# Kernel tuning notes

Measured on AMD Instinct MI355X. Metric: run time of the kernel, lower is better.

Reference implementation:

```python
import jax, jax.numpy as jnp
import numpy as np

T_TOK, N_UNITS, E, H, L_PATH, N_PATHS, B, VOCAB = 16, 4096, 128, 128, 32, 1024, 8, 16384
MAX_PATH_LEN = 32
PAD_ID = 0


def _run_lstm(x, Wi, Wh, b):
    # x: [T, N, E]; torch gate order i, f, g, o
    Hh = Wh.shape[1]
    h0 = jnp.zeros((x.shape[1], Hh), x.dtype)
    def step(carry, xt):
        h, c = carry
        g = xt @ Wi.T + h @ Wh.T + b
        i, f, gg, o = jnp.split(g, 4, axis=-1)
        c = jax.nn.sigmoid(f) * c + jax.nn.sigmoid(i) * jnp.tanh(gg)
        h = jax.nn.sigmoid(o) * jnp.tanh(c)
        return (h, c), h
    _, ys = jax.lax.scan(step, (h0, h0), x)
    return ys


def _bilstm(x, lengths, Wif, Whf, bf, Wib, Whb, bb):
    # emulates pack_padded_sequence + bidirectional LSTM + pad_packed (zeros past length)
    T = x.shape[0]
    t = jnp.arange(T)[:, None]
    valid = t < lengths[None, :]
    out_f = _run_lstm(x, Wif, Whf, bf)
    rev = jnp.clip(lengths[None, :] - 1 - t, 0, T - 1)  # reverse within each valid prefix
    x_rev = jnp.take_along_axis(x, rev[:, :, None], axis=0)
    out_b = jnp.take_along_axis(_run_lstm(x_rev, Wib, Whb, bb), rev[:, :, None], axis=0)
    return jnp.concatenate([out_f, out_b], axis=-1) * valid[:, :, None]


def _layernorm(x, g, b):
    m = x.mean(-1, keepdims=True)
    v = ((x - m) ** 2).mean(-1, keepdims=True)
    return (x - m) * jax.lax.rsqrt(v + 1e-5) * g + b


def _forward(units, paths, unit_per_data, path_per_data, emb, tl_Wif, tl_Whf, tl_bf,
             tl_Wib, tl_Whb, tl_bb, lin_W, lin_b, ln_g, ln_b, attn_w, attn_b,
             pl_Wif, pl_Whf, pl_bf, pl_Wib, pl_Whb, pl_bb, ul_W, ul_b):
    # ---- _token_encoder ----
    is_pad = units == PAD_ID
    tok_len = jnp.where(is_pad.any(0), jnp.argmax(is_pad, 0), units.shape[0])
    x = emb[units]                                              # [T, NU, E]
    h = _bilstm(x, tok_len, tl_Wif, tl_Whf, tl_bf, tl_Wib, tl_Whb, tl_bb)  # [T, NU, 2H]
    out = h @ lin_W.T + lin_b                                   # [T, NU, E]
    q = jnp.tanh(_layernorm(out, ln_g, ln_b))
    scores = q @ attn_w.T + attn_b                              # [T, NU, 1] local attention
    scores = jnp.where(is_pad[:, :, None], -1e9, scores)
    w = jax.nn.softmax(scores, axis=0)
    tok_feat = jnp.einsum('tn,tne->ne', w[..., 0], out)         # [NU, E]
    # ---- _unit_to_path (vectorized ragged gather) ----
    Lp, Pn = paths.shape
    has_end = (paths == -1).any(0)
    fe = jnp.where(has_end, jnp.argmax(paths == -1, 0), Lp)
    ML = min(Lp, MAX_PATH_LEN)
    nb = unit_per_data.shape[0]
    data_of_path = jnp.repeat(jnp.arange(nb), path_per_data, total_repeat_length=Pn)
    u_off = jnp.cumsum(unit_per_data) - unit_per_data
    off_p = u_off[data_of_path]
    un_p = unit_per_data[data_of_path]
    pL = paths[:ML]
    t = jnp.arange(ML)[:, None]
    within = t < fe[None, :]
    keep = within & (pL >= 0) & (pL < un_p[None, :])
    gidx = jnp.clip(jnp.clip(pL, 0, None) + off_p[None, :], 0, tok_feat.shape[0] - 1)
    feats = tok_feat[gidx] * keep[:, :, None]                   # [ML, P, E]
    mask = jnp.where(within, (pL < 0) | (pL > un_p[None, :]), True)
    # ---- _path_encoder ----
    p_len = jnp.where(mask.any(0), jnp.argmax(mask, 0), ML)
    hp = _bilstm(feats, p_len, pl_Wif, pl_Whf, pl_bf, pl_Wib, pl_Whb, pl_bb)
    return hp @ ul_W.T + ul_b                                   # [ML, P, E]


def setup_inputs() -> dict:
    rng = np.random.default_rng(0)
    tok_len = rng.integers(4, T_TOK + 1, N_UNITS); tok_len[0] = T_TOK
    units = rng.integers(1, VOCAB, (T_TOK, N_UNITS))
    units = np.where(np.arange(T_TOK)[:, None] < tok_len[None, :], units, PAD_ID)
    upd = N_UNITS // B
    p_len = rng.integers(8, L_PATH + 1, N_PATHS); p_len[0] = L_PATH
    paths = rng.integers(0, upd, (L_PATH, N_PATHS))
    paths = np.where(np.arange(L_PATH)[:, None] < p_len[None, :], paths, -1)
    key = jax.random.key(0)
    ks = iter(jax.random.split(key, 24))
    def pn(shape, s=0.08):
        return (jax.random.normal(next(ks), shape) * s).astype(jnp.float32)
    return dict(
        units=jnp.asarray(units, jnp.int32),
        paths=jnp.asarray(paths, jnp.int32),
        unit_per_data=jnp.full((B,), upd, jnp.int32),
        path_per_data=jnp.full((B,), N_PATHS // B, jnp.int32),
        emb=pn((VOCAB, E)),
        tl_Wif=pn((4 * H, E)), tl_Whf=pn((4 * H, H)), tl_bf=pn((4 * H,)),
        tl_Wib=pn((4 * H, E)), tl_Whb=pn((4 * H, H)), tl_bb=pn((4 * H,)),
        lin_W=pn((E, 2 * H)), lin_b=pn((E,)),
        ln_g=jnp.ones((E,), jnp.float32), ln_b=jnp.zeros((E,), jnp.float32),
        attn_w=pn((1, E)), attn_b=pn((1,)),
        pl_Wif=pn((4 * H, E)), pl_Whf=pn((4 * H, H)), pl_bf=pn((4 * H,)),
        pl_Wib=pn((4 * H, E)), pl_Whb=pn((4 * H, H)), pl_bb=pn((4 * H,)),
        ul_W=pn((E, 2 * H)), ul_b=pn((E,)),
    )


def reference(units, paths, unit_per_data, path_per_data, emb, tl_Wif, tl_Whf, tl_bf,
              tl_Wib, tl_Whb, tl_bb, lin_W, lin_b, ln_g, ln_b, attn_w, attn_b,
              pl_Wif, pl_Whf, pl_bf, pl_Wib, pl_Whb, pl_bb, ul_W, ul_b):
    return _forward(units, paths, unit_per_data, path_per_data, emb, tl_Wif, tl_Whf, tl_bf,
                    tl_Wib, tl_Whb, tl_bb, lin_W, lin_b, ln_g, ln_b, attn_w, attn_b,
                    pl_Wif, pl_Whf, pl_bf, pl_Wib, pl_Whb, pl_bb, ul_W, ul_b)
```

## Files before the change

kernel.cpp:

```cpp
#include <hip/hip_runtime.h>
#include <cstdint>
#include <cstddef>

#define T_TOKN 16
#define NUNITS 4096
#define LPATH  32
#define NPATHS 1024
#define BNUM   8

typedef __attribute__((ext_vector_type(8))) short short8;
typedef __attribute__((ext_vector_type(4))) short short4x;
typedef __attribute__((ext_vector_type(4))) float f32x4;

enum : size_t {
  OFF_WFRAG   = 0,
  OFF_LINFRAG = 262144,
  OFF_OUTF    = 294912,
  OFF_OUTB    = OFF_OUTF + 4194304,
  OFF_OUTLIN  = OFF_OUTB + 4194304,
  OFF_SCORES  = OFF_OUTLIN + 8388608,
  OFF_TOKFEAT = OFF_SCORES + 65536,
  OFF_POUTF   = OFF_TOKFEAT + 524288,
  OFF_POUTB   = OFF_POUTF + 2097152,
  OFF_INT     = OFF_POUTB + 2097152,
  WS_FLOATS   = OFF_INT + 8192
};

static __device__ __forceinline__ unsigned short f2bf(float f) {
  union { float f; unsigned u; } v; v.f = f;
  unsigned r = v.u + 0x7fffu + ((v.u >> 16) & 1u);
  return (unsigned short)(r >> 16);
}
static __device__ __forceinline__ unsigned pack_bf(float a, float b) {
  return (unsigned)f2bf(a) | ((unsigned)f2bf(b) << 16);
}
static __device__ __forceinline__ float sigf(float x)      { return 1.f / (1.f + __expf(-x)); }
static __device__ __forceinline__ float tanhfast(float x)  { return 2.f / (1.f + __expf(-2.f * x)) - 1.f; }

__global__ void prep_kernel(
    const float* __restrict__ tWif, const float* __restrict__ tWhf,
    const float* __restrict__ tWib, const float* __restrict__ tWhb,
    const float* __restrict__ pWif, const float* __restrict__ pWhf,
    const float* __restrict__ pWib, const float* __restrict__ pWhb,
    const float* __restrict__ linW, const float* __restrict__ ulW,
    const int* __restrict__ units, const int* __restrict__ paths,
    const int* __restrict__ upd, const int* __restrict__ ppd,
    float* __restrict__ ws, int* __restrict__ ip)
{
  int idx = blockIdx.x * 256 + threadIdx.x;
  if (idx < 524288) {
    unsigned short* wf = (unsigned short*)(ws + OFF_WFRAG);
    int mat = idx >> 17, rem = idx & 131071;
    int i  = rem & 7;
    int lane = (rem >> 3) & 63;
    int ct = (rem >> 9) & 3;
    int ks = (rem >> 11) & 7;
    int wv = (rem >> 14) & 7;
    int g = wv * 64 + ct * 16 + (lane & 15);
    int k = ks * 32 + ((lane >> 4) << 3) + i;
    const float* Wi; const float* Wh;
    switch (mat) {
      case 0: Wi = tWif; Wh = tWhf; break;
      case 1: Wi = tWib; Wh = tWhb; break;
      case 2: Wi = pWif; Wh = pWhf; break;
      default: Wi = pWib; Wh = pWhb; break;
    }
    float v = (k < 128) ? Wi[g * 128 + k] : Wh[g * 128 + (k - 128)];
    wf[idx] = f2bf(v);
  } else if (idx < 524288 + 65536) {
    unsigned short* lf = (unsigned short*)(ws + OFF_LINFRAG);
    int i2 = idx - 524288;
    int mat = i2 >> 15, rem = i2 & 32767;
    int i  = rem & 7;
    int lane = (rem >> 3) & 63;
    int ks = (rem >> 9) & 7;
    int ct = (rem >> 12) & 7;
    int e = ct * 16 + (lane & 15);
    int k = ks * 32 + ((lane >> 4) << 3) + i;
    const float* W = mat ? ulW : linW;
    lf[i2] = f2bf(W[e * 256 + k]);
  } else if (idx < 589824 + 4096) {
    int n = idx - 589824;
    int len = T_TOKN;
    for (int t = 0; t < T_TOKN; ++t)
      if (units[t * NUNITS + n] == 0) { len = t; break; }
    ip[n] = len;
  } else if (idx < 589824 + 5120) {
    int p = idx - (589824 + 4096);
    int* fe_a  = ip + 4096;
    int* p_len = ip + 5120;
    int* off_p = ip + 6144;
    int* un_p  = ip + 7168;
    int cum = 0; int d = BNUM - 1;
    for (int dd = 0; dd < BNUM; ++dd) {
      int c2 = cum + ppd[dd];
      if (p < c2) { d = dd; break; }
      cum = c2;
    }
    int off = 0;
    for (int dd = 0; dd < d; ++dd) off += upd[dd];
    int un = upd[d];
    off_p[p] = off; un_p[p] = un;
    int f = LPATH;
    for (int t = 0; t < LPATH; ++t)
      if (paths[t * NPATHS + p] == -1) { f = t; break; }
    fe_a[p] = f;
    int pl = LPATH;
    for (int t = 0; t < LPATH; ++t) {
      int v = paths[t * NPATHS + p];
      if ((t >= f) || (v < 0) || (v > un)) { pl = t; break; }
    }
    p_len[p] = pl;
  }
}

template <int MODE>
__global__ __launch_bounds__(1024, 4) void lstm_kernel(
    const unsigned short* __restrict__ wfragAll,
    const float* __restrict__ biasF, const float* __restrict__ biasB,
    const float* __restrict__ src,
    const int* __restrict__ idxsrc,
    const int* __restrict__ lens,
    const int* __restrict__ fe_a, const int* __restrict__ off_p, const int* __restrict__ un_p,
    unsigned short* __restrict__ outF, unsigned short* __restrict__ outB)
{
  constexpr int NN   = MODE ? NPATHS : NUNITS;
  constexpr int TT   = MODE ? LPATH : T_TOKN;
  constexpr int M    = MODE ? 8 : 32;
  constexpr int MR   = MODE ? 16 : 32;
  constexpr int NRT  = MR / 16;
  constexpr int ASTR = 264;
  constexpr int GSTR = 514;

  __shared__ unsigned short ash[MR * ASTR];
  __shared__ float gates[MR * GSTR];
  __shared__ int   idxL[M * TT];

  int tid  = threadIdx.x;
  int dir  = blockIdx.y;
  int n0   = blockIdx.x * M;
  int lane = tid & 63, wv = tid >> 6;

  const unsigned short* wbase =
      wfragAll + (size_t)((MODE ? 2 : 0) + dir) * 131072;
  int wv8 = wv >> 1;
  short8 bfr[8][2];
#pragma unroll
  for (int ks = 0; ks < 8; ++ks)
#pragma unroll
    for (int c2 = 0; c2 < 2; ++c2) {
      int ct = ((wv & 1) << 1) | c2;
      bfr[ks][c2] = *(const short8*)&wbase[((((wv8 * 8 + ks) * 4 + ct) * 64) + lane) * 8];
    }

  if (MODE == 0) {
    for (int i = tid; i < MR * 128; i += 1024)
      ash[(i >> 7) * ASTR + 128 + (i & 127)] = 0;
  } else {
    for (int i = tid; i < MR * ASTR; i += 1024) ash[i] = 0;
  }
  for (int i = tid; i < M * TT; i += 1024) {
    int u = i / TT, tt = i - u * TT;
    idxL[i] = idxsrc[tt * NN + (n0 + u)];
  }

  const float* bcp = dir ? biasB : biasF;
  int j2 = MODE ? (tid & 127) : ((tid & 63) * 2);
  int ug = MODE ? (tid >> 7)  : (tid >> 6);
  float2 b2[4];
#pragma unroll
  for (int q = 0; q < 4; ++q) {
    if (MODE == 0) b2[q] = *(const float2*)&bcp[q * 128 + j2];
    else           b2[q] = make_float2(bcp[q * 128 + j2], 0.f);
  }
  constexpr int NU = MODE ? 1 : 2;
  float cst0[NU], cst1[NU];
  int   ulen[NU];
  unsigned hp_prev[NU];
#pragma unroll
  for (int i = 0; i < NU; ++i) {
    cst0[i] = 0.f; cst1[i] = 0.f;
    ulen[i] = lens[n0 + ug * NU + i];
    hp_prev[i] = 0u;
  }

  int gu, gk0;
  if (MODE == 0) { gu = tid >> 5; gk0 = (tid & 31) * 4; }
  else           { gu = tid >> 7; gk0 = tid & 127; }
  int gn = n0 + gu;
  int glen = lens[gn];
  int gfe = 0, goff = 0, gun = 0;
  if (MODE) { gfe = fe_a[gn]; goff = off_p[gn]; gun = un_p[gn]; }

  float4 xq; float xs;
  __syncthreads();

  {
    int tau = dir ? min(max(glen - 1, 0), TT - 1) : 0;
    int v = idxL[gu * TT + tau];
    if (MODE == 0) {
      xq = *(const float4*)&src[(size_t)v * 128 + gk0];
    } else {
      bool keep = (tau < gfe) && (v >= 0) && (v < gun);
      xs = keep ? src[(size_t)min(v + goff, NUNITS - 1) * 128 + gk0] : 0.f;
    }
  }
  if (MODE == 0) {
    short4x x4;
    x4[0] = (short)f2bf(xq.x); x4[1] = (short)f2bf(xq.y);
    x4[2] = (short)f2bf(xq.z); x4[3] = (short)f2bf(xq.w);
    *(short4x*)&ash[gu * ASTR + gk0] = x4;
  } else {
    ash[gu * ASTR + gk0] = f2bf(xs);
  }
  __syncthreads();

#pragma unroll 1
  for (int t = 0; t < TT; ++t) {
    if (t > 0) {
      int tpw = t - 1;
#pragma unroll
      for (int i = 0; i < NU; ++i) {
        int u = ug * NU + i, n = n0 + u, L = ulen[i];
        bool vld = tpw < L;
        if (MODE == 0) {
          if (dir == 0) {
            *(unsigned*)&outF[((size_t)tpw * NN + n) * 128 + j2] = hp_prev[i];
          } else {
            size_t tr = vld ? (size_t)(L - 1 - tpw) : (size_t)tpw;
            *(unsigned*)&outB[(tr * NN + n) * 128 + j2] = vld ? hp_prev[i] : 0u;
          }
        } else {
          unsigned short hb = (unsigned short)hp_prev[i];
          if (dir == 0) {
            outF[((size_t)tpw * NN + n) * 128 + j2] = hb;
          } else {
            size_t tr = vld ? (size_t)(L - 1 - tpw) : (size_t)tpw;
            outB[(tr * NN + n) * 128 + j2] = vld ? hb : (unsigned short)0;
          }
        }
      }
    }
    {
      int tn = (t + 1 < TT) ? t + 1 : t;
      int taun = dir ? min(max(glen - 1 - tn, 0), TT - 1) : tn;
      int vn = idxL[gu * TT + taun];
      if (MODE == 0) {
        xq = *(const float4*)&src[(size_t)vn * 128 + gk0];
      } else {
        bool keep = (taun < gfe) && (vn >= 0) && (vn < gun);
        xs = keep ? src[(size_t)min(vn + goff, NUNITS - 1) * 128 + gk0] : 0.f;
      }
    }
    {
      f32x4 acc[NRT][2];
#pragma unroll
      for (int rt = 0; rt < NRT; ++rt)
#pragma unroll
        for (int c2 = 0; c2 < 2; ++c2) {
          f32x4 z = {0.f, 0.f, 0.f, 0.f};
          acc[rt][c2] = z;
        }
#pragma unroll
      for (int ks = 0; ks < 8; ++ks) {
        short8 afr[NRT];
#pragma unroll
        for (int rt = 0; rt < NRT; ++rt)
          afr[rt] = *(const short8*)&ash[(rt * 16 + (lane & 15)) * ASTR + ks * 32 + ((lane >> 4) << 3)];
#pragma unroll
        for (int rt = 0; rt < NRT; ++rt)
#pragma unroll
          for (int c2 = 0; c2 < 2; ++c2)
            acc[rt][c2] = __builtin_amdgcn_mfma_f32_16x16x32_bf16(
                afr[rt], bfr[ks][c2], acc[rt][c2], 0, 0, 0);
      }
#pragma unroll
      for (int rt = 0; rt < NRT; ++rt)
#pragma unroll
        for (int c2 = 0; c2 < 2; ++c2) {
          int g = wv * 32 + c2 * 16 + (lane & 15);
#pragma unroll
          for (int r = 0; r < 4; ++r) {
            int u = rt * 16 + ((lane >> 4) << 2) + r;
            gates[u * GSTR + g] = acc[rt][c2][r];
          }
        }
    }
    __syncthreads();

#pragma unroll
    for (int i = 0; i < NU; ++i) {
      int u = ug * NU + i;
      int L = ulen[i];
      if (t < L) {
        if (MODE == 0) {
          float2 g0 = *(const float2*)&gates[u * GSTR + j2];
          float2 g1 = *(const float2*)&gates[u * GSTR + 128 + j2];
          float2 g2 = *(const float2*)&gates[u * GSTR + 256 + j2];
          float2 g3 = *(const float2*)&gates[u * GSTR + 384 + j2];
          float i0 = sigf(g0.x + b2[0].x), i1 = sigf(g0.y + b2[0].y);
          float f0 = sigf(g1.x + b2[1].x), f1 = sigf(g1.y + b2[1].y);
          float c0 = tanhfast(g2.x + b2[2].x), c1 = tanhfast(g2.y + b2[2].y);
          float o0 = sigf(g3.x + b2[3].x), o1 = sigf(g3.y + b2[3].y);
          float cA = f0 * cst0[i] + i0 * c0;
          float cB = f1 * cst1[i] + i1 * c1;
          cst0[i] = cA; cst1[i] = cB;
          unsigned hp = pack_bf(o0 * tanhfast(cA), o1 * tanhfast(cB));
          *(unsigned*)&ash[u * ASTR + 128 + j2] = hp;
          hp_prev[i] = hp;
        } else {
          float p0 = gates[u * GSTR + j2]       + b2[0].x;
          float p1 = gates[u * GSTR + 128 + j2] + b2[1].x;
          float p2 = gates[u * GSTR + 256 + j2] + b2[2].x;
          float p3 = gates[u * GSTR + 384 + j2] + b2[3].x;
          float ig = sigf(p0), fg = sigf(p1), gg = tanhfast(p2), og = sigf(p3);
          float c = fg * cst0[i] + ig * gg;
          cst0[i] = c;
          unsigned short hb = f2bf(og * tanhfast(c));
          ash[u * ASTR + 128 + j2] = hb;
          hp_prev[i] = (unsigned)hb;
        }
      } else {
        hp_prev[i] = 0u;
      }
    }
    if (t + 1 < TT) {
      if (MODE == 0) {
        short4x x4;
        x4[0] = (short)f2bf(xq.x); x4[1] = (short)f2bf(xq.y);
        x4[2] = (short)f2bf(xq.z); x4[3] = (short)f2bf(xq.w);
        *(short4x*)&ash[gu * ASTR + gk0] = x4;
      } else {
        ash[gu * ASTR + gk0] = f2bf(xs);
      }
    }
    __syncthreads();
  }

  {
    int tpw = TT - 1;
#pragma unroll
    for (int i = 0; i < NU; ++i) {
      int u = ug * NU + i, n = n0 + u, L = ulen[i];
      bool vld = tpw < L;
      if (MODE == 0) {
        if (dir == 0) {
          *(unsigned*)&outF[((size_t)tpw * NN + n) * 128 + j2] = hp_prev[i];
        } else {
          size_t tr = vld ? (size_t)(L - 1 - tpw) : (size_t)tpw;
          *(unsigned*)&outB[(tr * NN + n) * 128 + j2] = vld ? hp_prev[i] : 0u;
        }
      } else {
        unsigned short hb = (unsigned short)hp_prev[i];
        if (dir == 0) {
          outF[((size_t)tpw * NN + n) * 128 + j2] = hb;
        } else {
          size_t tr = vld ? (size_t)(L - 1 - tpw) : (size_t)tpw;
          outB[(tr * NN + n) * 128 + j2] = vld ? hb : (unsigned short)0;
        }
      }
    }
  }
}

template <int EPI>
__global__ __launch_bounds__(256) void gemm_mfma(
    const unsigned short* __restrict__ INf, const unsigned short* __restrict__ INb,
    const int* __restrict__ lens,
    const unsigned short* __restrict__ Bfrag, const float* __restrict__ bias,
    float* __restrict__ OUT, float* __restrict__ scores,
    const float* __restrict__ lng, const float* __restrict__ lnb,
    const float* __restrict__ attw, const float* __restrict__ attb,
    const int* __restrict__ units, int Nn)
{
  constexpr int OSTR = 132;
  __shared__ float outs[64 * OSTR];
  __shared__ float red1[256];
  __shared__ float red2[256];
  __shared__ float rowm[64], rowr[64];
  __shared__ float awsh[128], lgsh[128], lbsh[128];

  int tid = threadIdx.x, lane = tid & 63, wv = tid >> 6;
  int row0 = blockIdx.x * 64;
  int t = row0 / Nn, n0 = row0 % Nn;

  if (EPI == 1 && tid < 128) {
    awsh[tid] = attw[tid]; lgsh[tid] = lng[tid]; lbsh[tid] = lnb[tid];
  }

  short8 bfr[8][2];
#pragma unroll
  for (int ks = 0; ks < 8; ++ks)
#pragma unroll
    for (int c2 = 0; c2 < 2; ++c2) {
      int ct = wv * 2 + c2;
      bfr[ks][c2] = *(const short8*)&Bfrag[(((ct * 8 + ks) * 64) + lane) * 8];
    }

  int rb = lane & 15;
  int koq = (lane >> 4) << 3;
  bool val[4];
#pragma unroll
  for (int rt = 0; rt < 4; ++rt)
    val[rt] = (EPI == 1) ? true : (t < lens[n0 + rt * 16 + rb]);

  f32x4 acc[4][2];
#pragma unroll
  for (int rt = 0; rt < 4; ++rt)
#pragma unroll
    for (int c2 = 0; c2 < 2; ++c2) {
      f32x4 z = {0.f, 0.f, 0.f, 0.f};
      acc[rt][c2] = z;
    }

#pragma unroll
  for (int ks = 0; ks < 8; ++ks) {
    const unsigned short* P = (ks < 4) ? INf : INb;
    int koff = (ks & 3) * 32 + koq;
#pragma unroll
    for (int rt = 0; rt < 4; ++rt) {
      short8 a = {0, 0, 0, 0, 0, 0, 0, 0};
      if (val[rt])
        a = *(const short8*)&P[((size_t)(row0 + rt * 16 + rb)) * 128 + koff];
#pragma unroll
      for (int c2 = 0; c2 < 2; ++c2)
        acc[rt][c2] = __builtin_amdgcn_mfma_f32_16x16x32_bf16(
            a, bfr[ks][c2], acc[rt][c2], 0, 0, 0);
    }
  }

  float bc[2];
#pragma unroll
  for (int c2 = 0; c2 < 2; ++c2) bc[c2] = bias[wv * 32 + c2 * 16 + rb];
#pragma unroll
  for (int rt = 0; rt < 4; ++rt)
#pragma unroll
    for (int c2 = 0; c2 < 2; ++c2) {
      int col = wv * 32 + c2 * 16 + rb;
      int ub  = rt * 16 + ((lane >> 4) << 2);
#pragma unroll
      for (int r = 0; r < 4; ++r)
        outs[(ub + r) * OSTR + col] = acc[rt][c2][r] + bc[c2];
    }
  __syncthreads();

  int row = tid >> 2, seg = tid & 3;
  const float* rp = &outs[row * OSTR + seg * 32];
  size_t go = ((size_t)(row0 + row)) * 128 + seg * 32;

  if (EPI == 0) {
#pragma unroll
    for (int x = 0; x < 8; ++x)
      *(f32x4*)&OUT[go + x * 4] = *(const f32x4*)&rp[x * 4];
  } else {
    f32x4 v[8];
    float s = 0.f, s2 = 0.f;
#pragma unroll
    for (int x = 0; x < 8; ++x) {
      v[x] = *(const f32x4*)&rp[x * 4];
#pragma unroll
      for (int c = 0; c < 4; ++c) { s += v[x][c]; s2 += v[x][c] * v[x][c]; }
    }
    red1[tid] = s; red2[tid] = s2;
    __syncthreads();
    if (tid < 64) {
      float a = red1[tid * 4] + red1[tid * 4 + 1] + red1[tid * 4 + 2] + red1[tid * 4 + 3];
      float b = red2[tid * 4] + red2[tid * 4 + 1] + red2[tid * 4 + 2] + red2[tid * 4 + 3];
      float m = a * (1.f / 128.f);
      float var = b * (1.f / 128.f) - m * m;
      rowm[tid] = m;
      rowr[tid] = rsqrtf(var + 1e-5f);
    }
    __syncthreads();
    float m = rowm[row], rs = rowr[row];
    float sp = 0.f;
#pragma unroll
    for (int x = 0; x < 8; ++x) {
#pragma unroll
      for (int c = 0; c < 4; ++c) {
        int col = seg * 32 + x * 4 + c;
        float q = tanhfast((v[x][c] - m) * rs * lgsh[col] + lbsh[col]);
        sp += q * awsh[col];
      }
      *(f32x4*)&OUT[go + x * 4] = v[x];
    }
    red1[tid] = sp;
    __syncthreads();
    if (tid < 64) {
      float s3 = red1[tid * 4] + red1[tid * 4 + 1] + red1[tid * 4 + 2] + red1[tid * 4 + 3]
               + attb[0];
      int n = n0 + tid;
      if (units[t * NUNITS + n] == 0) s3 = -1e9f;
      scores[t * NUNITS + n] = s3;
    }
  }
}

__global__ __launch_bounds__(128) void softmax_feat_kernel(
    const float* __restrict__ scores, const float* __restrict__ out_lin,
    float* __restrict__ tok_feat)
{
  int n = blockIdx.x;
  int e = threadIdx.x;
  float s[T_TOKN];
  float m = -1e30f;
#pragma unroll
  for (int t = 0; t < T_TOKN; ++t) { s[t] = scores[t * NUNITS + n]; m = fmaxf(m, s[t]); }
  float sum = 0.f;
#pragma unroll
  for (int t = 0; t < T_TOKN; ++t) { s[t] = expf(s[t] - m); sum += s[t]; }
  float inv = 1.f / sum;
  float a = 0.f;
#pragma unroll
  for (int t = 0; t < T_TOKN; ++t)
    a += s[t] * inv * out_lin[((size_t)t * NUNITS + n) * 128 + e];
  tok_feat[n * 128 + e] = a;
}

extern "C" void kernel_launch(void* const* d_in, const int* in_sizes, int n_in,
                              void* d_out, int out_size, void* d_ws, size_t ws_size,
                              hipStream_t stream)
{
  const int*   units = (const int*)d_in[0];
  const int*   paths = (const int*)d_in[1];
  const int*   upd   = (const int*)d_in[2];
  const int*   ppd   = (const int*)d_in[3];
  const float* emb   = (const float*)d_in[4];
  const float* tWif  = (const float*)d_in[5];
  const float* tWhf  = (const float*)d_in[6];
  const float* tbf   = (const float*)d_in[7];
  const float* tWib  = (const float*)d_in[8];
  const float* tWhb  = (const float*)d_in[9];
  const float* tbb   = (const float*)d_in[10];
  const float* linW  = (const float*)d_in[11];
  const float* linb  = (const float*)d_in[12];
  const float* lng   = (const float*)d_in[13];
  const float* lnb   = (const float*)d_in[14];
  const float* attw  = (const float*)d_in[15];
  const float* attb  = (const float*)d_in[16];
  const float* pWif  = (const float*)d_in[17];
  const float* pWhf  = (const float*)d_in[18];
  const float* pbf   = (const float*)d_in[19];
  const float* pWib  = (const float*)d_in[20];
  const float* pWhb  = (const float*)d_in[21];
  const float* pbb   = (const float*)d_in[22];
  const float* ulW   = (const float*)d_in[23];
  const float* ulb   = (const float*)d_in[24];

  float* ws = (float*)d_ws;
  int*   ip = (int*)(ws + OFF_INT);
  if (ws_size < WS_FLOATS * sizeof(float)) return;

  unsigned short* wfrag   = (unsigned short*)(ws + OFF_WFRAG);
  unsigned short* linfrag = (unsigned short*)(ws + OFF_LINFRAG);
  unsigned short* ulfrag  = linfrag + 32768;
  unsigned short* OUTF  = (unsigned short*)(ws + OFF_OUTF);
  unsigned short* OUTB  = (unsigned short*)(ws + OFF_OUTB);
  unsigned short* POUTF = (unsigned short*)(ws + OFF_POUTF);
  unsigned short* POUTB = (unsigned short*)(ws + OFF_POUTB);

  prep_kernel<<<2324, 256, 0, stream>>>(tWif, tWhf, tWib, tWhb,
                                        pWif, pWhf, pWib, pWhb,
                                        linW, ulW, units, paths, upd, ppd,
                                        ws, ip);

  lstm_kernel<0><<<dim3(128, 2), 1024, 0, stream>>>(
      wfrag, tbf, tbb, emb, units, ip , nullptr, nullptr, nullptr,
      OUTF, OUTB);

  gemm_mfma<1><<<1024, 256, 0, stream>>>(
      OUTF, OUTB, ip , linfrag, linb,
      ws + OFF_OUTLIN, ws + OFF_SCORES, lng, lnb, attw, attb, units, NUNITS);

  softmax_feat_kernel<<<4096, 128, 0, stream>>>(ws + OFF_SCORES, ws + OFF_OUTLIN,
                                                ws + OFF_TOKFEAT);

  lstm_kernel<1><<<dim3(128, 2), 1024, 0, stream>>>(
      wfrag, pbf, pbb, ws + OFF_TOKFEAT, paths, ip + 5120 ,
      ip + 4096 , ip + 6144 , ip + 7168 ,
      POUTF, POUTB);

  gemm_mfma<0><<<512, 256, 0, stream>>>(
      POUTF, POUTB, ip + 5120 , ulfrag, ulb,
      (float*)d_out, nullptr, nullptr, nullptr, nullptr, nullptr, nullptr, NPATHS);
}
```

Baseline: 317.7 us.

## Store linear output as bf16, write LSTM outputs immediately, move x-prefetch after MFMA

The intermediate token linear output is now stored as bf16 instead of fp32, halving the traffic between the GEMM epilogue and the softmax-feature kernel, which now converts back on load. The LSTM kernel writes each hidden state to global memory in the step that computes it rather than delaying the write by one step through a register. The next-step input prefetch is moved after the MFMA loop so the global load overlaps differently with the matrix work. The bf16 storage lowers the precision of the attention-weighted token features.

Result: faster. 306.2 us (-3.6%).

```diff
diff --git a/kernel.cpp b/kernel.cpp
--- a/kernel.cpp
+++ b/kernel.cpp
@@ -30,6 +30,10 @@
   union { float f; unsigned u; } v; v.f = f;
   unsigned r = v.u + 0x7fffu + ((v.u >> 16) & 1u);
   return (unsigned short)(r >> 16);
+}
+static __device__ __forceinline__ float bf2f(unsigned short u) {
+  union { unsigned u; float f; } v; v.u = ((unsigned)u) << 16;
+  return v.f;
 }
 static __device__ __forceinline__ unsigned pack_bf(float a, float b) {
   return (unsigned)f2bf(a) | ((unsigned)f2bf(b) << 16);
@@ -176,12 +180,10 @@
   constexpr int NU = MODE ? 1 : 2;
   float cst0[NU], cst1[NU];
   int   ulen[NU];
-  unsigned hp_prev[NU];
 #pragma unroll
   for (int i = 0; i < NU; ++i) {
     cst0[i] = 0.f; cst1[i] = 0.f;
     ulen[i] = lens[n0 + ug * NU + i];
-    hp_prev[i] = 0u;
   }
 
   int gu, gk0;
@@ -217,63 +219,37 @@
 
 #pragma unroll 1
   for (int t = 0; t < TT; ++t) {
-    if (t > 0) {
-      int tpw = t - 1;
-#pragma unroll
-      for (int i = 0; i < NU; ++i) {
-        int u = ug * NU + i, n = n0 + u, L = ulen[i];
-        bool vld = tpw < L;
-        if (MODE == 0) {
-          if (dir == 0) {
-            *(unsigned*)&outF[((size_t)tpw * NN + n) * 128 + j2] = hp_prev[i];
-          } else {
-            size_t tr = vld ? (size_t)(L - 1 - tpw) : (size_t)tpw;
-            *(unsigned*)&outB[(tr * NN + n) * 128 + j2] = vld ? hp_prev[i] : 0u;
-          }
-        } else {
-          unsigned short hb = (unsigned short)hp_prev[i];
-          if (dir == 0) {
-            outF[((size_t)tpw * NN + n) * 128 + j2] = hb;
-          } else {
-            size_t tr = vld ? (size_t)(L - 1 - tpw) : (size_t)tpw;
-            outB[(tr * NN + n) * 128 + j2] = vld ? hb : (unsigned short)0;
-          }
-        }
-      }
-    }
     {
       int tn = (t + 1 < TT) ? t + 1 : t;
       int taun = dir ? min(max(glen - 1 - tn, 0), TT - 1) : tn;
       int vn = idxL[gu * TT + taun];
+      f32x4 acc[NRT][2];
+#pragma unroll
+      for (int rt = 0; rt < NRT; ++rt)
+#pragma unroll
+        for (int c2 = 0; c2 < 2; ++c2) {
+          f32x4 z = {0.f, 0.f, 0.f, 0.f};
+          acc[rt][c2] = z;
+        }
+#pragma unroll
+      for (int ks = 0; ks < 8; ++ks) {
+        short8 afr[NRT];
+#pragma unroll
+        for (int rt = 0; rt < NRT; ++rt)
+          afr[rt] = *(const short8*)&ash[(rt * 16 + (lane & 15)) * ASTR + ks * 32 + ((lane >> 4) << 3)];
+#pragma unroll
+        for (int rt = 0; rt < NRT; ++rt)
+#pragma unroll
+          for (int c2 = 0; c2 < 2; ++c2)
+            acc[rt][c2] = __builtin_amdgcn_mfma_f32_16x16x32_bf16(
+                afr[rt], bfr[ks][c2], acc[rt][c2], 0, 0, 0);
+      }
       if (MODE == 0) {
         xq = *(const float4*)&src[(size_t)vn * 128 + gk0];
       } else {
         bool keep = (taun < gfe) && (vn >= 0) && (vn < gun);
         xs = keep ? src[(size_t)min(vn + goff, NUNITS - 1) * 128 + gk0] : 0.f;
       }
-    }
-    {
-      f32x4 acc[NRT][2];
-#pragma unroll
-      for (int rt = 0; rt < NRT; ++rt)
-#pragma unroll
-        for (int c2 = 0; c2 < 2; ++c2) {
-          f32x4 z = {0.f, 0.f, 0.f, 0.f};
-          acc[rt][c2] = z;
-        }
-#pragma unroll
-      for (int ks = 0; ks < 8; ++ks) {
-        short8 afr[NRT];
-#pragma unroll
-        for (int rt = 0; rt < NRT; ++rt)
-          afr[rt] = *(const short8*)&ash[(rt * 16 + (lane & 15)) * ASTR + ks * 32 + ((lane >> 4) << 3)];
-#pragma unroll
-        for (int rt = 0; rt < NRT; ++rt)
-#pragma unroll
-          for (int c2 = 0; c2 < 2; ++c2)
-            acc[rt][c2] = __builtin_amdgcn_mfma_f32_16x16x32_bf16(
-                afr[rt], bfr[ks][c2], acc[rt][c2], 0, 0, 0);
-      }
 #pragma unroll
       for (int rt = 0; rt < NRT; ++rt)
 #pragma unroll
@@ -291,6 +267,7 @@
 #pragma unroll
     for (int i = 0; i < NU; ++i) {
       int u = ug * NU + i;
+      int n = n0 + u;
       int L = ulen[i];
       if (t < L) {
         if (MODE == 0) {
@@ -307,7 +284,11 @@
           cst0[i] = cA; cst1[i] = cB;
           unsigned hp = pack_bf(o0 * tanhfast(cA), o1 * tanhfast(cB));
           *(unsigned*)&ash[u * ASTR + 128 + j2] = hp;
-          hp_prev[i] = hp;
+          if (dir == 0) {
+            *(unsigned*)&outF[((size_t)t * NN + n) * 128 + j2] = hp;
+          } else {
+            *(unsigned*)&outB[((size_t)(L - 1 - t) * NN + n) * 128 + j2] = hp;
+          }
         } else {
           float p0 = gates[u * GSTR + j2]       + b2[0].x;
           float p1 = gates[u * GSTR + 128 + j2] + b2[1].x;
@@ -318,10 +299,17 @@
           cst0[i] = c;
           unsigned short hb = f2bf(og * tanhfast(c));
           ash[u * ASTR + 128 + j2] = hb;
-          hp_prev[i] = (unsigned)hb;
+          if (dir == 0) outF[((size_t)t * NN + n) * 128 + j2] = hb;
+          else          outB[((size_t)(L - 1 - t) * NN + n) * 128 + j2] = hb;
         }
       } else {
-        hp_prev[i] = 0u;
+        if (MODE == 0) {
+          if (dir == 0) *(unsigned*)&outF[((size_t)t * NN + n) * 128 + j2] = 0u;
+          else          *(unsigned*)&outB[((size_t)t * NN + n) * 128 + j2] = 0u;
+        } else {
+          if (dir == 0) outF[((size_t)t * NN + n) * 128 + j2] = 0;
+          else          outB[((size_t)t * NN + n) * 128 + j2] = 0;
+        }
       }
     }
     if (t + 1 < TT) {
@@ -336,31 +324,6 @@
     }
     __syncthreads();
   }
-
-  {
-    int tpw = TT - 1;
-#pragma unroll
-    for (int i = 0; i < NU; ++i) {
-      int u = ug * NU + i, n = n0 + u, L = ulen[i];
-      bool vld = tpw < L;
-      if (MODE == 0) {
-        if (dir == 0) {
-          *(unsigned*)&outF[((size_t)tpw * NN + n) * 128 + j2] = hp_prev[i];
-        } else {
-          size_t tr = vld ? (size_t)(L - 1 - tpw) : (size_t)tpw;
-          *(unsigned*)&outB[(tr * NN + n) * 128 + j2] = vld ? hp_prev[i] : 0u;
-        }
-      } else {
-        unsigned short hb = (unsigned short)hp_prev[i];
-        if (dir == 0) {
-          outF[((size_t)tpw * NN + n) * 128 + j2] = hb;
-        } else {
-          size_t tr = vld ? (size_t)(L - 1 - tpw) : (size_t)tpw;
-          outB[(tr * NN + n) * 128 + j2] = vld ? hb : (unsigned short)0;
-        }
-      }
-    }
-  }
 }
 
 template <int EPI>
@@ -368,7 +331,7 @@
     const unsigned short* __restrict__ INf, const unsigned short* __restrict__ INb,
     const int* __restrict__ lens,
     const unsigned short* __restrict__ Bfrag, const float* __restrict__ bias,
-    float* __restrict__ OUT, float* __restrict__ scores,
+    void* __restrict__ OUTv, float* __restrict__ scores,
     const float* __restrict__ lng, const float* __restrict__ lnb,
     const float* __restrict__ attw, const float* __restrict__ attb,
     const int* __restrict__ units, int Nn)
@@ -449,10 +412,12 @@
   size_t go = ((size_t)(row0 + row)) * 128 + seg * 32;
 
   if (EPI == 0) {
+    float* OUT = (float*)OUTv;
 #pragma unroll
     for (int x = 0; x < 8; ++x)
       *(f32x4*)&OUT[go + x * 4] = *(const f32x4*)&rp[x * 4];
   } else {
+    unsigned short* OUT = (unsigned short*)OUTv;
     f32x4 v[8];
     float s = 0.f, s2 = 0.f;
 #pragma unroll
@@ -476,13 +441,15 @@
     float sp = 0.f;
 #pragma unroll
     for (int x = 0; x < 8; ++x) {
+      short4x pv;
 #pragma unroll
       for (int c = 0; c < 4; ++c) {
         int col = seg * 32 + x * 4 + c;
         float q = tanhfast((v[x][c] - m) * rs * lgsh[col] + lbsh[col]);
         sp += q * awsh[col];
+        pv[c] = (short)f2bf(v[x][c]);
       }
-      *(f32x4*)&OUT[go + x * 4] = v[x];
+      *(short4x*)&OUT[go + x * 4] = pv;
     }
     red1[tid] = sp;
     __syncthreads();
@@ -497,7 +464,7 @@
 }
 
 __global__ __launch_bounds__(128) void softmax_feat_kernel(
-    const float* __restrict__ scores, const float* __restrict__ out_lin,
+    const float* __restrict__ scores, const unsigned short* __restrict__ out_lin,
     float* __restrict__ tok_feat)
 {
   int n = blockIdx.x;
@@ -513,7 +480,7 @@
   float a = 0.f;
 #pragma unroll
   for (int t = 0; t < T_TOKN; ++t)
-    a += s[t] * inv * out_lin[((size_t)t * NUNITS + n) * 128 + e];
+    a += s[t] * inv * bf2f(out_lin[((size_t)t * NUNITS + n) * 128 + e]);
   tok_feat[n * 128 + e] = a;
 }
 
@@ -570,10 +537,11 @@
 
   gemm_mfma<1><<<1024, 256, 0, stream>>>(
       OUTF, OUTB, ip , linfrag, linb,
-      ws + OFF_OUTLIN, ws + OFF_SCORES, lng, lnb, attw, attb, units, NUNITS);
-
-  softmax_feat_kernel<<<4096, 128, 0, stream>>>(ws + OFF_SCORES, ws + OFF_OUTLIN,
-                                                ws + OFF_TOKFEAT);
+      (void*)(ws + OFF_OUTLIN), ws + OFF_SCORES, lng, lnb, attw, attb, units, NUNITS);
+
+  softmax_feat_kernel<<<4096, 128, 0, stream>>>(
+      ws + OFF_SCORES, (const unsigned short*)(ws + OFF_OUTLIN),
+      ws + OFF_TOKFEAT);
 
   lstm_kernel<1><<<dim3(128, 2), 1024, 0, stream>>>(
       wfrag, pbf, pbb, ws + OFF_TOKFEAT, paths, ip + 5120 ,
@@ -582,5 +550,5 @@
 
   gemm_mfma<0><<<512, 256, 0, stream>>>(
       POUTF, POUTB, ip + 5120 , ulfrag, ulb,
-      (float*)d_out, nullptr, nullptr, nullptr, nullptr, nullptr, nullptr, NPATHS);
-}
+      (void*)d_out, nullptr, nullptr, nullptr, nullptr, nullptr, nullptr, NPATHS);
+}
```
